# Kernel optimization log

Hardware: AMD Instinct MI355X
Metric: run time of the kernel (lower is better)

The kernel has to match this reference:

```python
import jax, jax.numpy as jnp
import numpy as np

B, MAX_NPUS, MEM_SIZE = 16, 1024, 4096
IN_SIZE, REG_SIZE, MEM_DIM = 512, 256, 128
GRU_IN = IN_SIZE + MEM_DIM
MMU_OUT = MEM_DIM * 5 + 4  # 644


def setup_inputs() -> dict:
    key = jax.random.key(0)
    ks = jax.random.split(key, 12)
    s = 0.02
    return {
        "input_vector": jax.random.normal(ks[0], (B, IN_SIZE), jnp.float32),
        "registers": jax.random.normal(ks[1], (B, MAX_NPUS, REG_SIZE), jnp.float32),
        "memory_context": jax.random.normal(ks[2], (B, MEM_SIZE, MEM_DIM), jnp.float32),
        "W_ih": jax.random.normal(ks[3], (3 * REG_SIZE, GRU_IN), jnp.float32) * s,
        "b_ih": jax.random.normal(ks[4], (3 * REG_SIZE,), jnp.float32) * s,
        "W_hh": jax.random.normal(ks[5], (3 * REG_SIZE, REG_SIZE), jnp.float32) * s,
        "b_hh": jax.random.normal(ks[6], (3 * REG_SIZE,), jnp.float32) * s,
        "W_mmu": jax.random.normal(ks[7], (MMU_OUT, REG_SIZE), jnp.float32) * s,
        "b_mmu": jax.random.normal(ks[8], (MMU_OUT,), jnp.float32) * s,
        "W_out": jax.random.normal(ks[9], (IN_SIZE, REG_SIZE), jnp.float32) * s,
        "b_out": jax.random.normal(ks[10], (IN_SIZE,), jnp.float32) * s,
        "active_npus": MAX_NPUS,
    }


def reference(input_vector, registers, memory_context, W_ih, b_ih, W_hh, b_hh,
              W_mmu, b_mmu, W_out, b_out, active_npus):
    md, rs = MEM_DIM, REG_SIZE
    curr = registers[:, :active_npus, :]                      # [B,N,rs]
    mmu = jnp.einsum('bnr,or->bno', curr, W_mmu) + b_mmu      # [B,N,5*md+4]
    query = mmu[..., :md]
    w_key = mmu[..., md:2 * md]
    w_val = mmu[..., 2 * md:3 * md]
    w_gate = jax.nn.sigmoid(mmu[..., 3 * md:3 * md + 1])
    ssd_key = mmu[..., 3 * md + 1:4 * md + 1]
    ssd_val = mmu[..., 4 * md + 1:5 * md + 1]
    ssd_gate = jax.nn.softmax(mmu[..., 5 * md + 1:5 * md + 4], axis=-1)
    # attention read over shared memory
    scores = jnp.einsum('bnd,bmd->bnm', query, memory_context) / jnp.sqrt(jnp.float32(md))
    attn = jax.nn.softmax(scores, axis=-1)                    # [B,N,M]
    read_data = jnp.einsum('bnm,bmd->bnd', attn, memory_context)
    # GRU cell (torch GRUCell semantics, gate order r,z,n)
    inp = jnp.broadcast_to(input_vector[:, None, :], (curr.shape[0], active_npus, input_vector.shape[-1]))
    x = jnp.concatenate([inp, read_data], axis=-1)            # [B,N,in+md]
    gi = jnp.einsum('bni,oi->bno', x, W_ih) + b_ih            # [B,N,3*rs]
    gh = jnp.einsum('bnr,or->bno', curr, W_hh) + b_hh
    gi_r, gi_z, gi_n = gi[..., :rs], gi[..., rs:2 * rs], gi[..., 2 * rs:]
    gh_r, gh_z, gh_n = gh[..., :rs], gh[..., rs:2 * rs], gh[..., 2 * rs:]
    r = jax.nn.sigmoid(gi_r + gh_r)
    z = jax.nn.sigmoid(gi_z + gh_z)
    n = jnp.tanh(gi_n + r * gh_n)
    new_regs = (1.0 - z) * n + z * curr                       # [B,N,rs]
    output_active = jnp.einsum('bnr,or->bno', new_regs, W_out) + b_out
    return (output_active, new_regs, w_key, w_val, w_gate, ssd_key, ssd_val, ssd_gate)
```

## Files before the change

kernel.cpp:

```cpp
#include <hip/hip_runtime.h>
#include <hip/hip_bf16.h>
#include <math.h>

#define B_      16
#define NPUS    1024
#define MEMS    4096
#define INS     512
#define RS      256
#define MD      128
#define GRUIN   640
#define MMUO    644
#define NROWS   (B_*NPUS)

#define O_OUT   0u
#define O_REGS  8388608u
#define O_WKEY  12582912u
#define O_WVAL  14680064u
#define O_WGATE 16777216u
#define O_SSDK  16793600u
#define O_SSDV  18890752u
#define O_SSDG  20987904u

typedef __attribute__((ext_vector_type(8))) short bf16x8;
typedef __attribute__((ext_vector_type(4))) float f32x4;
typedef __attribute__((ext_vector_type(4))) unsigned short u16x4;

__device__ __forceinline__ float sigf(float x){ return 1.f/(1.f+__expf(-x)); }
__device__ __forceinline__ unsigned short bfu(float x){
    __hip_bfloat16 h = __float2bfloat16(x);
    return __builtin_bit_cast(unsigned short, h);
}
__device__ __forceinline__ float b2f(unsigned short u){
    unsigned v = ((unsigned)u) << 16;
    return __builtin_bit_cast(float, v);
}
__device__ __forceinline__ void gload16(const void* g, void* s)
{
    __builtin_amdgcn_global_load_lds(
        (const __attribute__((address_space(1))) void*)g,
        (__attribute__((address_space(3))) void*)s, 16, 0, 0);
}

__global__ __launch_bounds__(256) void k_cvt(const float* __restrict__ src,
                                             unsigned short* __restrict__ dst, int n4)
{
    int i = blockIdx.x*256 + threadIdx.x;
    if (i >= n4) return;
    float4 v = ((const float4*)src)[i];
    u16x4 o = { bfu(v.x), bfu(v.y), bfu(v.z), bfu(v.w) };
    ((u16x4*)dst)[i] = o;
}

__global__ __launch_bounds__(256) void k_cvt5g(const float* __restrict__ s0, unsigned short* __restrict__ d0,
                                               const float* __restrict__ s1, unsigned short* __restrict__ d1,
                                               const float* __restrict__ s2, unsigned short* __restrict__ d2,
                                               const float* __restrict__ s3, unsigned short* __restrict__ d3,
                                               const float* __restrict__ s4, unsigned short* __restrict__ d4,
                                               float* __restrict__ gi0)
{
    __shared__ float xs[INS];
    if (blockIdx.x >= 969) {
        const int gb = blockIdx.x - 969;
        const int b = gb / 3, seg = gb % 3;
        const int t = threadIdx.x;
        for (int i = t; i < INS; i += 256) xs[i] = s4[(size_t)b*INS + i];
        __syncthreads();
        const int o = seg*256 + t;
        const float* wrow = s1 + (size_t)o*GRUIN;
        float a0 = 0.f, a1 = 0.f, a2 = 0.f, a3 = 0.f;
        for (int k = 0; k < INS; k += 4) {
            float4 wv = *(const float4*)(wrow + k);
            a0 += xs[k]*wv.x; a1 += xs[k+1]*wv.y; a2 += xs[k+2]*wv.z; a3 += xs[k+3]*wv.w;
        }
        gi0[(size_t)b*768 + o] = (a0 + a1) + (a2 + a3);
        return;
    }
    int gi = blockIdx.x*256 + threadIdx.x;
    const float* s; unsigned short* d; int idx;
    if      (gi < 41216)  { s = s0; d = d0; idx = gi; }
    else if (gi < 164096) { s = s1; d = d1; idx = gi - 41216; }
    else if (gi < 213248) { s = s2; d = d2; idx = gi - 164096; }
    else if (gi < 246016) { s = s3; d = d3; idx = gi - 213248; }
    else                  { s = s4; d = d4; idx = gi - 246016; }
    float4 v = ((const float4*)s)[idx];
    u16x4 o = { bfu(v.x), bfu(v.y), bfu(v.z), bfu(v.w) };
    ((u16x4*)d)[idx] = o;
}

__global__ __launch_bounds__(256) void k_conv(const float* __restrict__ mem,
                                              __hip_bfloat16* __restrict__ memB,
                                              __hip_bfloat16* __restrict__ memT)
{
    __shared__ float Ms[32][129];
    const int t = threadIdx.x;
    const int b = blockIdx.x >> 7;
    const int m0 = (blockIdx.x & 127) << 5;
    const float* src = mem + ((size_t)b*MEMS + m0)*MD;
    for (int idx = t; idx < 32*128; idx += 256) {
        int m = idx >> 7, d = idx & 127;
        float v = src[(size_t)m*MD + d];
        Ms[m][d] = v;
        memB[((size_t)b*MEMS + m0 + m)*MD + d] = __float2bfloat16(v);
    }
    __syncthreads();
    for (int idx = t; idx < 128*32; idx += 256) {
        int d = idx >> 5, m = idx & 31;
        int pos = (m < 16) ? (2*m) : (2*(m-16)+1);
        memT[((size_t)b*MD + d)*MEMS + m0 + pos] = __float2bfloat16(Ms[m][d]);
    }
}

__global__ __launch_bounds__(256, 4) void k_mmu(const __hip_bfloat16* __restrict__ Ab,
                                                const __hip_bfloat16* __restrict__ Wb,
                                                const float* __restrict__ bias,
                                                float* __restrict__ out,
                                                __hip_bfloat16* __restrict__ qbf)
{
    __shared__ __hip_bfloat16 At[2][64][32];
    __shared__ __hip_bfloat16 Bt[2][128][32];
    const int t = threadIdx.x, w = t >> 6, l = t & 63;
    const int lg = l >> 4, ll = l & 15;
    const int m0 = blockIdx.x*64;
    const int n0 = blockIdx.y*128;
    f32x4 acc[8];
    #pragma unroll
    for (int c = 0; c < 8; c++) acc[c] = (f32x4){0,0,0,0};

    const char* aSrc;
    {
        int row = t >> 2, cc = t & 3;
        int gc = cc ^ ((row >> 1) & 3);
        aSrc = (const char*)((const short*)Ab + (size_t)(m0+row)*RS) + gc*16;
    }
    const char* bSrc[2];
    #pragma unroll
    for (int j = 0; j < 2; j++) {
        int ci = w*128 + j*64 + l;
        int row = ci >> 2, cc = ci & 3;
        int gc = cc ^ ((row >> 1) & 3);
        bSrc[j] = (const char*)((const short*)Wb + (size_t)(n0+row)*RS) + gc*16;
    }

    auto stage = [&](int buf, int it) {
        int off = it*64;
        char* abase = (char*)(&At[buf][0][0]) + (size_t)(w << 6)*16;
        gload16(aSrc + off, abase);
        #pragma unroll
        for (int j = 0; j < 2; j++) {
            char* bbase = (char*)(&Bt[buf][0][0]) + (size_t)(w*128 + j*64)*16;
            gload16(bSrc[j] + off, bbase);
        }
    };

    stage(0, 0);
    asm volatile("s_waitcnt vmcnt(0)" ::: "memory");
    __syncthreads();
    int cur = 0;
    const int arow = (w << 4) + ll;
    const int aswz = ((lg ^ ((arow >> 1) & 3)) << 4);
    for (int it = 0; it < 8; ++it) {
        if (it + 1 < 8) stage(cur ^ 1, it + 1);
        const char* ab = (const char*)(&At[cur][0][0]);
        const char* bb = (const char*)(&Bt[cur][0][0]);
        bf16x8 af = *(const bf16x8*)(ab + arow*64 + aswz);
        #pragma unroll
        for (int c = 0; c < 8; c++) {
            int r0 = c*16 + ll;
            int sw = ((lg ^ ((r0 >> 1) & 3)) << 4);
            bf16x8 bf = *(const bf16x8*)(bb + (size_t)r0*64 + sw);
            acc[c] = __builtin_amdgcn_mfma_f32_16x16x32_bf16(af, bf, acc[c], 0, 0, 0);
        }
        asm volatile("s_waitcnt vmcnt(0)" ::: "memory");
        __syncthreads();
        cur ^= 1;
    }
    const int wm0 = m0 + (w << 4);
    #pragma unroll
    for (int c = 0; c < 8; c++) {
        int o = n0 + c*16 + ll;
        if (o > 640) continue;
        float bv = bias[o];
        #pragma unroll
        for (int r = 0; r < 4; r++) {
            int row = wm0 + lg*4 + r;
            float v = acc[c][r] + bv;
            if      (o < MD)        qbf[(size_t)row*MD + o] = __float2bfloat16(v * 0.08838834764831845f);
            else if (o < 2*MD)      out[O_WKEY + (size_t)row*MD + (o -   MD)] = v;
            else if (o < 3*MD)      out[O_WVAL + (size_t)row*MD + (o - 2*MD)] = v;
            else if (o == 3*MD)     out[O_WGATE + row] = sigf(v);
            else if (o < 4*MD + 1)  out[O_SSDK + (size_t)row*MD + (o - (3*MD+1))] = v;
            else                    out[O_SSDV + (size_t)row*MD + (o - (4*MD+1))] = v;
        }
    }
    if (n0 == 640) {
        #pragma unroll
        for (int r = 0; r < 4; r++) {
            int o = n0 + ll;
            float vr = acc[0][r] + ((o < MMUO) ? bias[o] : 0.f);
            float va = __shfl(vr, lg*16 + 1);
            float vb = __shfl(vr, lg*16 + 2);
            float vc = __shfl(vr, lg*16 + 3);
            float mm = fmaxf(va, fmaxf(vb, vc));
            float ea = __expf(va-mm), eb = __expf(vb-mm), ec = __expf(vc-mm);
            float inv = 1.f/(ea+eb+ec);
            int row = wm0 + lg*4 + r;
            if (ll == 1) out[O_SSDG + (size_t)row*3 + 0] = ea*inv;
            if (ll == 2) out[O_SSDG + (size_t)row*3 + 1] = eb*inv;
            if (ll == 3) out[O_SSDG + (size_t)row*3 + 2] = ec*inv;
        }
    }
}

__global__ __launch_bounds__(256, 2) void k_attn(const __hip_bfloat16* __restrict__ qb,
                                                 const __hip_bfloat16* __restrict__ memB,
                                                 const __hip_bfloat16* __restrict__ memT,
                                                 unsigned short* __restrict__ Opart,
                                                 float* __restrict__ MLpart)
{
    __shared__ __hip_bfloat16 Kt[2][32][128];
    __shared__ __hip_bfloat16 Vt[2][128][32];
    __shared__ unsigned int Pl32[4][16][20];
    const int t = threadIdx.x, w = t >> 6, l = t & 63;
    const int lg = l >> 4, ll = l & 15;
    const int bid = blockIdx.x;
    const int xcd = bid & 7, rest = bid >> 3;
    const int b = xcd + ((rest >> 5) << 3);
    const int sub = rest & 31;
    const int qblk = sub >> 2, kh = sub & 3;
    const int qrow0 = (b << 10) + (qblk << 7) + (w << 5);
    const int k_beg = kh << 10;
    const float THR = 4.0f;

    const short* Q = (const short*)qb;
    bf16x8 qf[2][4];
    #pragma unroll
    for (int qs = 0; qs < 2; qs++)
        #pragma unroll
        for (int ks = 0; ks < 4; ks++)
            qf[qs][ks] = *(const bf16x8*)(Q + (size_t)(qrow0 + qs*16 + ll)*MD + ks*32 + lg*8);

    f32x4 O[2][8];
    #pragma unroll
    for (int qs = 0; qs < 2; qs++)
        #pragma unroll
        for (int dt = 0; dt < 8; dt++) O[qs][dt] = (f32x4){0.f,0.f,0.f,0.f};
    float m_run[2][4], lsum[2][4];
    #pragma unroll
    for (int qs = 0; qs < 2; qs++)
        #pragma unroll
        for (int r = 0; r < 4; r++) { m_run[qs][r] = -INFINITY; lsum[qs][r] = 0.f; }

    const char* MbB = (const char*)memB + (size_t)b*MEMS*MD*2;
    const char* MtB = (const char*)memT + (size_t)b*MD*MEMS*2;

    auto stage = [&](int buf, int it) {
        const int k0 = k_beg + it*32;
        char* kbase = (char*)(&Kt[buf][0][0]);
        char* vbase = (char*)(&Vt[buf][0][0]);
        #pragma unroll
        for (int j = 0; j < 2; j++) {
            int ci = (w << 7) + (j << 6) + l;
            int krow = ci >> 4, cc = ci & 15;
            int gc = cc ^ (krow & 7);
            gload16(MbB + (size_t)(k0 + krow)*256 + gc*16,
                    kbase + (size_t)((w << 7) + (j << 6))*16);
        }
        #pragma unroll
        for (int j = 0; j < 2; j++) {
            int ci = (w << 7) + (j << 6) + l;
            int drow = ci >> 2, cc = ci & 3;
            int gc = cc ^ ((drow >> 1) & 3);
            gload16(MtB + (size_t)drow*(MEMS*2) + (size_t)k0*2 + gc*16,
                    vbase + (size_t)((w << 7) + (j << 6))*16);
        }
    };

    stage(0, 0);
    asm volatile("s_waitcnt vmcnt(0)" ::: "memory");
    asm volatile("s_barrier" ::: "memory");
    int cur = 0;
    const int NIT = 1024/32;
    const int vsw = ((lg ^ ((ll >> 1) & 3)) << 4);
    for (int it = 0; it < NIT; ++it) {
        if (it + 1 < NIT) {
            stage(cur ^ 1, it + 1);
            asm volatile("s_waitcnt vmcnt(4)" ::: "memory");
        } else {
            asm volatile("s_waitcnt vmcnt(0)" ::: "memory");
        }
        asm volatile("s_barrier" ::: "memory");
        const char* kbase = (const char*)(&Kt[cur][0][0]);
        const char* vbase = (const char*)(&Vt[cur][0][0]);
        bf16x8 vf[8];
        #pragma unroll
        for (int dt = 0; dt < 8; dt++)
            vf[dt] = *(const bf16x8*)(vbase + (size_t)(dt*16 + ll)*64 + vsw);
        f32x4 s[2][2];
        s[0][0]=(f32x4){0,0,0,0}; s[0][1]=(f32x4){0,0,0,0};
        s[1][0]=(f32x4){0,0,0,0}; s[1][1]=(f32x4){0,0,0,0};
        #pragma unroll
        for (int ks = 0; ks < 4; ks++) {
            int c0 = ks*4 + lg;
            int sw = (c0 ^ (ll & 7)) << 4;
            bf16x8 kf0 = *(const bf16x8*)(kbase + (size_t)ll*256 + sw);
            bf16x8 kf1 = *(const bf16x8*)(kbase + (size_t)(16 + ll)*256 + sw);
            s[0][0] = __builtin_amdgcn_mfma_f32_16x16x32_bf16(qf[0][ks], kf0, s[0][0], 0, 0, 0);
            s[1][0] = __builtin_amdgcn_mfma_f32_16x16x32_bf16(qf[1][ks], kf0, s[1][0], 0, 0, 0);
            s[0][1] = __builtin_amdgcn_mfma_f32_16x16x32_bf16(qf[0][ks], kf1, s[0][1], 0, 0, 0);
            s[1][1] = __builtin_amdgcn_mfma_f32_16x16x32_bf16(qf[1][ks], kf1, s[1][1], 0, 0, 0);
        }
        bool need = false;
        #pragma unroll
        for (int qs = 0; qs < 2; qs++)
            #pragma unroll
            for (int r = 0; r < 4; r++) {
                need |= (s[qs][0][r] > m_run[qs][r] + THR);
                need |= (s[qs][1][r] > m_run[qs][r] + THR);
            }
        if (__any(need)) {
            #pragma unroll
            for (int qs = 0; qs < 2; qs++)
                #pragma unroll
                for (int r = 0; r < 4; r++) {
                    float v = fmaxf(s[qs][0][r], s[qs][1][r]);
                    v = fmaxf(v, __shfl_xor(v, 1));
                    v = fmaxf(v, __shfl_xor(v, 2));
                    v = fmaxf(v, __shfl_xor(v, 4));
                    v = fmaxf(v, __shfl_xor(v, 8));
                    float mnew = fmaxf(m_run[qs][r], v);
                    float alpha = __expf(m_run[qs][r] - mnew);
                    m_run[qs][r] = mnew;
                    lsum[qs][r] *= alpha;
                    #pragma unroll
                    for (int dt = 0; dt < 8; dt++) O[qs][dt][r] *= alpha;
                }
        }
        #pragma unroll
        for (int qs = 0; qs < 2; qs++) {
            #pragma unroll
            for (int r = 0; r < 4; r++) {
                float p0 = __expf(s[qs][0][r] - m_run[qs][r]);
                float p1 = __expf(s[qs][1][r] - m_run[qs][r]);
                Pl32[w][lg*4 + r][ll] = (unsigned)bfu(p0) | ((unsigned)bfu(p1) << 16);
                lsum[qs][r] += p0 + p1;
            }
            __builtin_amdgcn_wave_barrier();
            bf16x8 pa = *(const bf16x8*)((const char*)(&Pl32[w][0][0]) + (size_t)ll*80 + lg*16);
            __builtin_amdgcn_wave_barrier();
            #pragma unroll
            for (int dt = 0; dt < 8; dt++)
                O[qs][dt] = __builtin_amdgcn_mfma_f32_16x16x32_bf16(pa, vf[dt], O[qs][dt], 0, 0, 0);
        }
        asm volatile("s_barrier" ::: "memory");
        cur ^= 1;
    }
    #pragma unroll
    for (int qs = 0; qs < 2; qs++)
        #pragma unroll
        for (int r = 0; r < 4; r++) {
            float s2 = lsum[qs][r];
            s2 += __shfl_xor(s2, 1);
            s2 += __shfl_xor(s2, 2);
            s2 += __shfl_xor(s2, 4);
            s2 += __shfl_xor(s2, 8);
            lsum[qs][r] = s2;
        }
    #pragma unroll
    for (int qs = 0; qs < 2; qs++)
        #pragma unroll
        for (int dt = 0; dt < 8; dt++)
            #pragma unroll
            for (int r = 0; r < 4; r++) {
                int row = qrow0 + qs*16 + lg*4 + r;
                Opart[((size_t)row*4 + kh)*128 + dt*16 + ll] = bfu(O[qs][dt][r]);
            }
    if (ll == 0) {
        #pragma unroll
        for (int qs = 0; qs < 2; qs++)
            #pragma unroll
            for (int r = 0; r < 4; r++) {
                int row = qrow0 + qs*16 + lg*4 + r;
                MLpart[((size_t)row*4 + kh)*2 + 0] = m_run[qs][r];
                MLpart[((size_t)row*4 + kh)*2 + 1] = lsum[qs][r];
            }
    }
}

__global__ __launch_bounds__(256) void k_comb(const unsigned short* __restrict__ Opart,
                                              const float* __restrict__ MLpart,
                                              __hip_bfloat16* __restrict__ rdb)
{
    const int t = threadIdx.x;
    const int row = blockIdx.x*64 + (t >> 2);
    const int c0 = (t & 3) * 32;
    float m[4], lv[4], a[4];
    float M = -INFINITY;
    #pragma unroll
    for (int i = 0; i < 4; i++) {
        m[i]  = MLpart[((size_t)row*4 + i)*2 + 0];
        lv[i] = MLpart[((size_t)row*4 + i)*2 + 1];
        M = fmaxf(M, m[i]);
    }
    float L = 0.f;
    #pragma unroll
    for (int i = 0; i < 4; i++) { a[i] = __expf(m[i] - M); L += a[i]*lv[i]; }
    float invL = 1.f / L;
    #pragma unroll
    for (int i = 0; i < 4; i++) a[i] *= invL;
    unsigned short* dst = (unsigned short*)rdb + (size_t)row*128 + c0;
    #pragma unroll
    for (int j = 0; j < 8; j++) {
        float acc0=0.f, acc1=0.f, acc2=0.f, acc3=0.f;
        #pragma unroll
        for (int i = 0; i < 4; i++) {
            u16x4 x = ((const u16x4*)(Opart + ((size_t)row*4 + i)*128 + c0))[j];
            acc0 += a[i]*b2f(x[0]); acc1 += a[i]*b2f(x[1]);
            acc2 += a[i]*b2f(x[2]); acc3 += a[i]*b2f(x[3]);
        }
        u16x4 o = { bfu(acc0), bfu(acc1), bfu(acc2), bfu(acc3) };
        ((u16x4*)dst)[j] = o;
    }
}

__global__ __launch_bounds__(256, 4) void k_gru(const float* __restrict__ gi0,
                                                const __hip_bfloat16* __restrict__ rdb,
                                                const __hip_bfloat16* __restrict__ regsb,
                                                const float* __restrict__ regs,
                                                const __hip_bfloat16* __restrict__ Wihb,
                                                const float* __restrict__ bih,
                                                const __hip_bfloat16* __restrict__ Whhb,
                                                const float* __restrict__ bhh,
                                                float* __restrict__ newregs,
                                                __hip_bfloat16* __restrict__ nregsb)
{
    __shared__ __hip_bfloat16 At[2][64][32];
    __shared__ __hip_bfloat16 Bt[2][192][32];
    const int t = threadIdx.x, w = t >> 6, l = t & 63;
    const int lg = l >> 4, ll = l & 15;
    const int m0 = blockIdx.x*64;
    const int n0 = blockIdx.y*64;
    const int batch = blockIdx.x >> 4;
    const short* Rd = (const short*)rdb;
    const short* Hb = (const short*)regsb;
    const short* Wi = (const short*)Wihb;
    const short* Wh = (const short*)Whhb;

    f32x4 aR[4], aZ[4], aNi[4], aNh[4];
    #pragma unroll
    for (int c = 0; c < 4; c++) {
        int o = n0 + c*16 + ll;
        float gR = gi0[(size_t)batch*768 + o];
        float gZ = gi0[(size_t)batch*768 + 256 + o];
        float gN = gi0[(size_t)batch*768 + 512 + o];
        aR[c]  = (f32x4){gR,gR,gR,gR};
        aZ[c]  = (f32x4){gZ,gZ,gZ,gZ};
        aNi[c] = (f32x4){gN,gN,gN,gN};
        aNh[c] = (f32x4){0,0,0,0};
    }

    const int aci = (w << 6) + l;
    const int arow_s = aci >> 2, acc_s = aci & 3;
    const int agc = acc_s ^ ((arow_s >> 1) & 3);
    const char* aSrcA = (const char*)(Rd + (size_t)(m0+arow_s)*MD) + agc*16;
    const char* aSrcB = (const char*)(Hb + (size_t)(m0+arow_s)*RS) + agc*16;
    const char* bSrcA0; const char* bSrcA1; const char* bSrcA2;
    const char* bSrcB0; const char* bSrcB1; const char* bSrcB2;
    {
        int ci, row, cc, gc, g, col;
        ci = w*192 + 0*64 + l; row = ci >> 2; cc = ci & 3; gc = cc ^ ((row >> 1) & 3);
        g = row >> 6; col = row & 63;
        bSrcA0 = (const char*)(Wi + (size_t)(g*RS + n0 + col)*GRUIN + INS) + gc*16;
        bSrcB0 = (const char*)(Wh + (size_t)(g*RS + n0 + col)*RS) + gc*16;
        ci = w*192 + 1*64 + l; row = ci >> 2; cc = ci & 3; gc = cc ^ ((row >> 1) & 3);
        g = row >> 6; col = row & 63;
        bSrcA1 = (const char*)(Wi + (size_t)(g*RS + n0 + col)*GRUIN + INS) + gc*16;
        bSrcB1 = (const char*)(Wh + (size_t)(g*RS + n0 + col)*RS) + gc*16;
        ci = w*192 + 2*64 + l; row = ci >> 2; cc = ci & 3; gc = cc ^ ((row >> 1) & 3);
        g = row >> 6; col = row & 63;
        bSrcA2 = (const char*)(Wi + (size_t)(g*RS + n0 + col)*GRUIN + INS) + gc*16;
        bSrcB2 = (const char*)(Wh + (size_t)(g*RS + n0 + col)*RS) + gc*16;
    }

    const int NITA = 4, NIT = 12;
    auto stage = [&](int buf, int it) {
        char* abase = (char*)(&At[buf][0][0]) + (size_t)(w << 6)*16;
        char* bbase = (char*)(&Bt[buf][0][0]) + (size_t)(w*192)*16;
        const char *as, *b0, *b1, *b2;
        if (it < NITA) {
            int off = it*64;
            as = aSrcA + off; b0 = bSrcA0 + off; b1 = bSrcA1 + off; b2 = bSrcA2 + off;
        } else {
            int off = (it - NITA)*64;
            as = aSrcB + off; b0 = bSrcB0 + off; b1 = bSrcB1 + off; b2 = bSrcB2 + off;
        }
        gload16(as, abase);
        gload16(b0, bbase);
        gload16(b1, bbase + 64*16);
        gload16(b2, bbase + 128*16);
    };

    stage(0, 0);
    asm volatile("s_waitcnt vmcnt(0)" ::: "memory");
    __syncthreads();
    int cur = 0;
    const int arow = (w << 4) + ll;
    const int aswz = ((lg ^ ((arow >> 1) & 3)) << 4);
    for (int it = 0; it < NIT; ++it) {
        if (it + 1 < NIT) stage(cur ^ 1, it + 1);
        const char* ab = (const char*)(&At[cur][0][0]);
        const char* bb = (const char*)(&Bt[cur][0][0]);
        bf16x8 af = *(const bf16x8*)(ab + arow*64 + aswz);
        if (it < NITA) {
            #pragma unroll
            for (int c = 0; c < 4; c++) {
                int r0 = c*16 + ll;
                int sw = ((lg ^ ((r0 >> 1) & 3)) << 4);
                bf16x8 bR = *(const bf16x8*)(bb + (size_t)r0*64 + sw);
                bf16x8 bZ = *(const bf16x8*)(bb + (size_t)(r0 + 64)*64 + sw);
                bf16x8 bN = *(const bf16x8*)(bb + (size_t)(r0 + 128)*64 + sw);
                aR[c]  = __builtin_amdgcn_mfma_f32_16x16x32_bf16(af, bR, aR[c],  0, 0, 0);
                aZ[c]  = __builtin_amdgcn_mfma_f32_16x16x32_bf16(af, bZ, aZ[c],  0, 0, 0);
                aNi[c] = __builtin_amdgcn_mfma_f32_16x16x32_bf16(af, bN, aNi[c], 0, 0, 0);
            }
        } else {
            #pragma unroll
            for (int c = 0; c < 4; c++) {
                int r0 = c*16 + ll;
                int sw = ((lg ^ ((r0 >> 1) & 3)) << 4);
                bf16x8 bR = *(const bf16x8*)(bb + (size_t)r0*64 + sw);
                bf16x8 bZ = *(const bf16x8*)(bb + (size_t)(r0 + 64)*64 + sw);
                bf16x8 bN = *(const bf16x8*)(bb + (size_t)(r0 + 128)*64 + sw);
                aR[c]  = __builtin_amdgcn_mfma_f32_16x16x32_bf16(af, bR, aR[c],  0, 0, 0);
                aZ[c]  = __builtin_amdgcn_mfma_f32_16x16x32_bf16(af, bZ, aZ[c],  0, 0, 0);
                aNh[c] = __builtin_amdgcn_mfma_f32_16x16x32_bf16(af, bN, aNh[c], 0, 0, 0);
            }
        }
        asm volatile("s_waitcnt vmcnt(0)" ::: "memory");
        __syncthreads();
        cur ^= 1;
    }
    const int wm0 = m0 + (w << 4);
    #pragma unroll
    for (int c = 0; c < 4; c++) {
        int o = n0 + c*16 + ll;
        float bR = bih[o]        + bhh[o];
        float bZ = bih[o +   RS] + bhh[o +   RS];
        float bNi = bih[o + 2*RS];
        float bNh = bhh[o + 2*RS];
        #pragma unroll
        for (int r = 0; r < 4; r++) {
            int row = wm0 + lg*4 + r;
            float rr = sigf(aR[c][r] + bR);
            float zz = sigf(aZ[c][r] + bZ);
            float nn = tanhf(aNi[c][r] + bNi + rr*(aNh[c][r] + bNh));
            float cv = regs[(size_t)row*RS + o];
            float nv = (1.f - zz)*nn + zz*cv;
            newregs[(size_t)row*RS + o] = nv;
            nregsb[(size_t)row*RS + o] = __float2bfloat16(nv);
        }
    }
}

__global__ __launch_bounds__(256, 4) void k_out(const __hip_bfloat16* __restrict__ Ab,
                                                const __hip_bfloat16* __restrict__ Wb,
                                                const float* __restrict__ bias,
                                                float* __restrict__ out0)
{
    __shared__ __hip_bfloat16 At[2][64][32];
    __shared__ __hip_bfloat16 Bt[2][128][32];
    const int t = threadIdx.x, w = t >> 6, l = t & 63;
    const int lg = l >> 4, ll = l & 15;
    const int m0 = blockIdx.x*64;
    const int n0 = blockIdx.y*128;
    f32x4 acc[8];
    #pragma unroll
    for (int c = 0; c < 8; c++) acc[c] = (f32x4){0,0,0,0};

    const char* aSrc;
    {
        int row = t >> 2, cc = t & 3;
        int gc = cc ^ ((row >> 1) & 3);
        aSrc = (const char*)((const short*)Ab + (size_t)(m0+row)*RS) + gc*16;
    }
    const char* bSrc[2];
    #pragma unroll
    for (int j = 0; j < 2; j++) {
        int ci = w*128 + j*64 + l;
        int row = ci >> 2, cc = ci & 3;
        int gc = cc ^ ((row >> 1) & 3);
        bSrc[j] = (const char*)((const short*)Wb + (size_t)(n0+row)*RS) + gc*16;
    }

    auto stage = [&](int buf, int it) {
        int off = it*64;
        char* abase = (char*)(&At[buf][0][0]) + (size_t)(w << 6)*16;
        gload16(aSrc + off, abase);
        #pragma unroll
        for (int j = 0; j < 2; j++) {
            char* bbase = (char*)(&Bt[buf][0][0]) + (size_t)(w*128 + j*64)*16;
            gload16(bSrc[j] + off, bbase);
        }
    };

    stage(0, 0);
    asm volatile("s_waitcnt vmcnt(0)" ::: "memory");
    __syncthreads();
    int cur = 0;
    const int arow = (w << 4) + ll;
    const int aswz = ((lg ^ ((arow >> 1) & 3)) << 4);
    for (int it = 0; it < 8; ++it) {
        if (it + 1 < 8) stage(cur ^ 1, it + 1);
        const char* ab = (const char*)(&At[cur][0][0]);
        const char* bb = (const char*)(&Bt[cur][0][0]);
        bf16x8 af = *(const bf16x8*)(ab + arow*64 + aswz);
        #pragma unroll
        for (int c = 0; c < 8; c++) {
            int r0 = c*16 + ll;
            int sw = ((lg ^ ((r0 >> 1) & 3)) << 4);
            bf16x8 bf = *(const bf16x8*)(bb + (size_t)r0*64 + sw);
            acc[c] = __builtin_amdgcn_mfma_f32_16x16x32_bf16(af, bf, acc[c], 0, 0, 0);
        }
        asm volatile("s_waitcnt vmcnt(0)" ::: "memory");
        __syncthreads();
        cur ^= 1;
    }
    const int wm0 = m0 + (w << 4);
    #pragma unroll
    for (int c = 0; c < 8; c++) {
        int o = n0 + c*16 + ll;
        float bv = bias[o];
        #pragma unroll
        for (int r = 0; r < 4; r++) {
            int row = wm0 + lg*4 + r;
            out0[(size_t)row*INS + o] = acc[c][r] + bv;
        }
    }
}

extern "C" void kernel_launch(void* const* d_in, const int* in_sizes, int n_in,
                              void* d_out, int out_size, void* d_ws, size_t ws_size,
                              hipStream_t stream)
{
    const float* inp  = (const float*)d_in[0];
    const float* regs = (const float*)d_in[1];
    const float* mem  = (const float*)d_in[2];
    const float* Wih  = (const float*)d_in[3];
    const float* bih  = (const float*)d_in[4];
    const float* Whh  = (const float*)d_in[5];
    const float* bhh  = (const float*)d_in[6];
    const float* Wmmu = (const float*)d_in[7];
    const float* bmmu = (const float*)d_in[8];
    const float* Wout = (const float*)d_in[9];
    const float* bout = (const float*)d_in[10];
    float* out = (float*)d_out;

    char* ws = (char*)d_ws;
    __hip_bfloat16* qbf    = (__hip_bfloat16*)(ws);
    __hip_bfloat16* rdb    = (__hip_bfloat16*)(ws + ((size_t)4<<20));
    __hip_bfloat16* memB   = (__hip_bfloat16*)(ws + ((size_t)8<<20));
    __hip_bfloat16* memT   = (__hip_bfloat16*)(ws + ((size_t)24<<20));
    __hip_bfloat16* regsb  = (__hip_bfloat16*)(ws + ((size_t)40<<20));
    __hip_bfloat16* nregsb = (__hip_bfloat16*)(ws + ((size_t)48<<20));
    __hip_bfloat16* Wmmub  = (__hip_bfloat16*)(ws + ((size_t)56<<20));
    __hip_bfloat16* Wihb   = (__hip_bfloat16*)(ws + ((size_t)56<<20) + ( 1<<20));
    __hip_bfloat16* Whhb   = (__hip_bfloat16*)(ws + ((size_t)56<<20) + ( 2<<20));
    __hip_bfloat16* Woutb  = (__hip_bfloat16*)(ws + ((size_t)56<<20) + ( 3<<20));
    __hip_bfloat16* inpb   = (__hip_bfloat16*)(ws + ((size_t)56<<20) + ( 4<<20));
    float*          MLpart = (float*)(ws + ((size_t)61<<20));
    float*          gi0    = (float*)(ws + ((size_t)61<<20) + (1<<19));
    unsigned short* Opart  = (unsigned short*)(out + O_OUT);

    k_cvt5g<<<1017, 256, 0, stream>>>(Wmmu, (unsigned short*)Wmmub,
                                      Wih,  (unsigned short*)Wihb,
                                      Whh,  (unsigned short*)Whhb,
                                      Wout, (unsigned short*)Woutb,
                                      inp,  (unsigned short*)inpb, gi0);
    k_cvt<<<(4194304/4 + 255)/256, 256, 0, stream>>>(regs, (unsigned short*)regsb, 4194304/4);
    k_conv<<<B_*128, 256, 0, stream>>>(mem, memB, memT);

    dim3 g1(NROWS/64, 6);
    k_mmu<<<g1, 256, 0, stream>>>(regsb, Wmmub, bmmu, out, qbf);
    k_attn<<<512, 256, 0, stream>>>(qbf, memB, memT, Opart, MLpart);
    k_comb<<<NROWS/64, 256, 0, stream>>>(Opart, MLpart, rdb);
    dim3 g3(NROWS/64, 4);
    k_gru<<<g3, 256, 0, stream>>>(gi0, rdb, regsb, regs, Wihb, bih, Whhb, bhh,
                                  out + O_REGS, nregsb);
    dim3 g4(NROWS/64, 4);
    k_out<<<g4, 256, 0, stream>>>(nregsb, Woutb, bout, out);
}
```

Before: 153.9 us.

## Triple-buffer attention K/V tiles and use exp2 with log2e-prescaled queries

```diff
diff --git a/kernel.cpp b/kernel.cpp
--- a/kernel.cpp
+++ b/kernel.cpp
@@ -33,6 +33,13 @@
 __device__ __forceinline__ float b2f(unsigned short u){
     unsigned v = ((unsigned)u) << 16;
     return __builtin_bit_cast(float, v);
+}
+__device__ __forceinline__ float ex2(float x){
+#if __has_builtin(__builtin_amdgcn_exp2f)
+    return __builtin_amdgcn_exp2f(x);
+#else
+    return exp2f(x);
+#endif
 }
 __device__ __forceinline__ void gload16(const void* g, void* s)
 {
@@ -175,6 +182,7 @@
         cur ^= 1;
     }
     const int wm0 = m0 + (w << 4);
+    const float QSCL = 0.08838834764831845f * 1.4426950408889634f;
     #pragma unroll
     for (int c = 0; c < 8; c++) {
         int o = n0 + c*16 + ll;
@@ -184,7 +192,7 @@
         for (int r = 0; r < 4; r++) {
             int row = wm0 + lg*4 + r;
             float v = acc[c][r] + bv;
-            if      (o < MD)        qbf[(size_t)row*MD + o] = __float2bfloat16(v * 0.08838834764831845f);
+            if      (o < MD)        qbf[(size_t)row*MD + o] = __float2bfloat16(v * QSCL);
             else if (o < 2*MD)      out[O_WKEY + (size_t)row*MD + (o -   MD)] = v;
             else if (o < 3*MD)      out[O_WVAL + (size_t)row*MD + (o - 2*MD)] = v;
             else if (o == 3*MD)     out[O_WGATE + row] = sigf(v);
@@ -217,8 +225,8 @@
                                                  unsigned short* __restrict__ Opart,
                                                  float* __restrict__ MLpart)
 {
-    __shared__ __hip_bfloat16 Kt[2][32][128];
-    __shared__ __hip_bfloat16 Vt[2][128][32];
+    __shared__ __hip_bfloat16 Kt[3][32][128];
+    __shared__ __hip_bfloat16 Vt[3][128][32];
     __shared__ unsigned int Pl32[4][16][20];
     const int t = threadIdx.x, w = t >> 6, l = t & 63;
     const int lg = l >> 4, ll = l & 15;
@@ -229,7 +237,7 @@
     const int qblk = sub >> 2, kh = sub & 3;
     const int qrow0 = (b << 10) + (qblk << 7) + (w << 5);
     const int k_beg = kh << 10;
-    const float THR = 4.0f;
+    const float THR = 5.77f;
 
     const short* Q = (const short*)qb;
     bf16x8 qf[2][4];
@@ -275,20 +283,17 @@
         }
     };
 
+    const int NIT = 1024/32;
     stage(0, 0);
-    asm volatile("s_waitcnt vmcnt(0)" ::: "memory");
-    asm volatile("s_barrier" ::: "memory");
+    stage(1, 1);
     int cur = 0;
-    const int NIT = 1024/32;
     const int vsw = ((lg ^ ((ll >> 1) & 3)) << 4);
     for (int it = 0; it < NIT; ++it) {
-        if (it + 1 < NIT) {
-            stage(cur ^ 1, it + 1);
-            asm volatile("s_waitcnt vmcnt(4)" ::: "memory");
-        } else {
-            asm volatile("s_waitcnt vmcnt(0)" ::: "memory");
-        }
+        if (it < NIT-1) { asm volatile("s_waitcnt vmcnt(4)" ::: "memory"); }
+        else            { asm volatile("s_waitcnt vmcnt(0)" ::: "memory"); }
         asm volatile("s_barrier" ::: "memory");
+        int st = cur + 2; if (st >= 3) st -= 3;
+        if (it + 2 < NIT) stage(st, it + 2);
         const char* kbase = (const char*)(&Kt[cur][0][0]);
         const char* vbase = (const char*)(&Vt[cur][0][0]);
         bf16x8 vf[8];
@@ -328,7 +333,7 @@
                     v = fmaxf(v, __shfl_xor(v, 4));
                     v = fmaxf(v, __shfl_xor(v, 8));
                     float mnew = fmaxf(m_run[qs][r], v);
-                    float alpha = __expf(m_run[qs][r] - mnew);
+                    float alpha = ex2(m_run[qs][r] - mnew);
                     m_run[qs][r] = mnew;
                     lsum[qs][r] *= alpha;
                     #pragma unroll
@@ -339,8 +344,8 @@
         for (int qs = 0; qs < 2; qs++) {
             #pragma unroll
             for (int r = 0; r < 4; r++) {
-                float p0 = __expf(s[qs][0][r] - m_run[qs][r]);
-                float p1 = __expf(s[qs][1][r] - m_run[qs][r]);
+                float p0 = ex2(s[qs][0][r] - m_run[qs][r]);
+                float p1 = ex2(s[qs][1][r] - m_run[qs][r]);
                 Pl32[w][lg*4 + r][ll] = (unsigned)bfu(p0) | ((unsigned)bfu(p1) << 16);
                 lsum[qs][r] += p0 + p1;
             }
@@ -351,8 +356,7 @@
             for (int dt = 0; dt < 8; dt++)
                 O[qs][dt] = __builtin_amdgcn_mfma_f32_16x16x32_bf16(pa, vf[dt], O[qs][dt], 0, 0, 0);
         }
-        asm volatile("s_barrier" ::: "memory");
-        cur ^= 1;
+        cur = (cur + 1 == 3) ? 0 : cur + 1;
     }
     #pragma unroll
     for (int qs = 0; qs < 2; qs++)
@@ -403,7 +407,7 @@
     }
     float L = 0.f;
     #pragma unroll
-    for (int i = 0; i < 4; i++) { a[i] = __expf(m[i] - M); L += a[i]*lv[i]; }
+    for (int i = 0; i < 4; i++) { a[i] = ex2(m[i] - M); L += a[i]*lv[i]; }
     float invL = 1.f / L;
     #pragma unroll
     for (int i = 0; i < 4; i++) a[i] *= invL;
```

Result: no change. 156.1 us (+1.4%).
